# Optimization experiments

Hardware: AMD Instinct MI355X
Metric: run time of the kernel (lower is better)

## Reference

```python
import jax, jax.numpy as jnp
import numpy as np

DECAY = 0.99
EPS = 1e-10
COMMIT = 0.25
K = 1024
D = 64


def setup_inputs() -> dict:
    key = jax.random.key(0)
    k1, k2, k3, k4 = jax.random.split(key, 4)
    return {
        "z_e": jax.random.normal(k1, (64, 64, 32, 32), dtype=jnp.float32),
        "embedding_w": jax.random.normal(k2, (K, D), dtype=jnp.float32),
        "ema_cluster_size": jax.random.uniform(k3, (K,), dtype=jnp.float32),
        "ema_w": jax.random.normal(k4, (K, D), dtype=jnp.float32),
    }


def reference(z_e, embedding_w, ema_cluster_size, ema_w):
    # [B, C, H, W] -> [B, H, W, C] -> [N, D]
    z_nhwc = jnp.transpose(z_e, (0, 2, 3, 1))
    z_flat = z_nhwc.reshape(-1, z_nhwc.shape[-1])

    # Squared-euclidean distances via ||z||^2 + ||e||^2 - 2 z e^T  -> [N, K]
    z_sq = jnp.sum(z_flat * z_flat, axis=1, keepdims=True)
    e_sq = jnp.sum(embedding_w * embedding_w, axis=1)
    distances = z_sq + e_sq - 2.0 * (z_flat @ embedding_w.T)

    indices = jnp.argmin(distances, axis=1)                      # [N]
    encodings = jax.nn.one_hot(indices, K, dtype=z_flat.dtype)   # [N, K]

    quantized = embedding_w[indices].reshape(z_nhwc.shape)       # [B, H, W, C]

    # --- EMA codebook update (training path; no-grad in original) ---
    counts = jnp.sum(encodings, axis=0)                          # [K]
    new_cluster_size = DECAY * ema_cluster_size + (1.0 - DECAY) * counts
    dw = encodings.T @ z_flat                                    # [K, D]
    new_ema_w = DECAY * ema_w + (1.0 - DECAY) * dw
    n = jnp.sum(new_cluster_size)
    cluster_size = (new_cluster_size + EPS) / (n + K * EPS) * n
    new_embedding_w = new_ema_w / cluster_size[:, None]

    # Commitment loss (quantized detached)
    diff = jax.lax.stop_gradient(quantized) - z_nhwc
    loss = COMMIT * jnp.mean(diff * diff)

    # Straight-through estimator
    quantized_st = z_nhwc + jax.lax.stop_gradient(quantized - z_nhwc)

    avg_probs = jnp.mean(encodings, axis=0)
    perplexity = jnp.exp(-jnp.sum(avg_probs * jnp.log(avg_probs + 1e-10)))

    quantized_out = jnp.transpose(quantized_st, (0, 3, 1, 2))    # [B, C, H, W]
    return (quantized_out, loss, perplexity, encodings,
            new_embedding_w, new_cluster_size, new_ema_w)
```

## Files before the change

### kernel.cpp

```cpp
#include <hip/hip_runtime.h>
#include <math.h>

#define NTOT 65536
#define KCB  1024
#define DIM  64

typedef float fvec2 __attribute__((ext_vector_type(2)));
typedef float fvec4 __attribute__((ext_vector_type(4)));
typedef short sh8  __attribute__((ext_vector_type(8)));

static const size_t OFF_Q    = 0;
static const size_t OFF_LOSS = 4194304;
static const size_t OFF_PERP = 4194305;
static const size_t OFF_ENC  = 4194306;
static const size_t OFF_EMB  = 71303170;
static const size_t OFF_NCS  = 71368706;
static const size_t OFF_NEMA = 71369730;

static const size_t WSO_IDX   = 0;
static const size_t WSO_ESQ   = 262144;
static const size_t WSO_LOSSP = 266240;
static const size_t WSO_CNT   = 270336;
static const size_t WSO_SCAL  = 274432;
static const size_t WSO_EBH   = 278528;
static const size_t WSO_EBL   = 409600;
static const size_t WSO_ZC    = 540672;
static const size_t WS_NEED_ZC = 540672 + (size_t)NTOT * DIM * 4;

__device__ __forceinline__ unsigned short f2bf(float f) {
    unsigned u = __builtin_bit_cast(unsigned, f);
    return (unsigned short)((u + 0x7FFFu + ((u >> 16) & 1u)) >> 16);
}
__device__ __forceinline__ float bf2f(unsigned short h) {
    unsigned u = ((unsigned)h) << 16;
    return __builtin_bit_cast(float, u);
}

__global__ void k_eprep(const float* __restrict__ emb,
                        unsigned short* __restrict__ ebh,
                        unsigned short* __restrict__ ebl,
                        float* __restrict__ esq) {
    int gid = blockIdx.x * 256 + threadIdx.x;
    int c = gid >> 3, ko8 = gid & 7;
    const fvec4* p = (const fvec4*)(emb + ((size_t)c << 6) + (ko8 << 3));
    fvec4 v0 = p[0], v1 = p[1];
    float f[8] = {v0.x, v0.y, v0.z, v0.w, v1.x, v1.y, v1.z, v1.w};
    sh8 h, l;
    float sq0 = 0.f, sq1 = 0.f;
#pragma unroll
    for (int j = 0; j < 8; ++j) {
        unsigned short hb = f2bf(f[j]);
        h[j] = (short)hb;
        l[j] = (short)f2bf(f[j] - bf2f(hb));
        if (j < 4) sq0 = fmaf(f[j], f[j], sq0); else sq1 = fmaf(f[j], f[j], sq1);
    }
    float sq = sq0 + sq1;
    sq += __shfl_xor(sq, 1, 64);
    sq += __shfl_xor(sq, 2, 64);
    sq += __shfl_xor(sq, 4, 64);
    if (ko8 == 0) esq[c] = sq;

    int ct = c >> 4, cl = c & 15, kc = ko8 >> 2, ko = ko8 & 3;
    size_t base = ((((size_t)ct << 1) + kc) << 9) + (((size_t)(ko << 4) + cl) << 3);
    *(sh8*)(ebh + base) = h;
    *(sh8*)(ebl + base) = l;
}

__global__ __launch_bounds__(256, 4)
void k_assign(const float* __restrict__ ze, const float* __restrict__ emb,
              const float* __restrict__ esq,
              const unsigned short* __restrict__ ebh,
              const unsigned short* __restrict__ ebl,
              int* __restrict__ idx_out, float* __restrict__ lossp,
              float* __restrict__ zc, int use_zc) {
    __shared__ float zt[4096];
    __shared__ __align__(16) float etq[4096];
    __shared__ int   sfidx[64];

    const int tid  = threadIdx.x;
    const int blk  = blockIdx.x;
    const int b    = blk >> 4;
    const int hw0  = (blk & 15) << 6;
    const int n0   = blk << 6;
    const int lane = tid & 63;
    const int wave = tid >> 6;
    const int cg   = lane & 15;
    const int ko   = lane >> 4;

    char*  ebuf0 = (char*)etq;
    char*  ebuf1 = (char*)etq + 4096;
    float* esql  = etq + 2048;

#pragma unroll
    for (int j = 0; j < 4; ++j) {
        int idx = tid + (j << 8);
        int d = idx >> 4, r0 = (idx & 15) << 2;
        const fvec4 v = *(const fvec4*)(ze + (((size_t)(b << 6) + d) << 10) + hw0 + r0);
        zt[(r0 + 0) * 64 + d] = v.x;
        zt[(r0 + 1) * 64 + d] = v.y;
        zt[(r0 + 2) * 64 + d] = v.z;
        zt[(r0 + 3) * 64 + d] = v.w;
    }
    {
        fvec4 e4 = *(const fvec4*)(esq + (tid << 2));
        *(fvec4*)&esql[tid << 2] = e4;
    }

    const unsigned short* sgbase = (tid < 128) ? ebh : ebl;
    const int soff   = (tid & 127) << 3;
    const int dstoff = (tid < 128) ? (tid << 4) : (2048 + ((tid - 128) << 4));
    const size_t lo  = (size_t)lane << 4;

#define TILE(i) ((((i) + (blk << 1)) & 63))

    sh8 stg = *(const sh8*)(sgbase + ((size_t)TILE(0) << 10) + soff);
    __syncthreads();

    const int arow = (wave << 4) + cg;
    sh8 Ah0, Ah1, Al0, Al1;
#pragma unroll
    for (int j = 0; j < 8; ++j) {
        float f0 = zt[arow * 64 + (ko << 3) + j];
        float f1 = zt[arow * 64 + 32 + (ko << 3) + j];
        unsigned short h0 = f2bf(f0), h1 = f2bf(f1);
        Ah0[j] = (short)h0;  Al0[j] = (short)f2bf(f0 - bf2f(h0));
        Ah1[j] = (short)h1;  Al1[j] = (short)f2bf(f1 - bf2f(h1));
    }

    *(sh8*)(ebuf0 + dstoff) = stg;
    __syncthreads();

    float tb[4]  = {3.4e38f, 3.4e38f, 3.4e38f, 3.4e38f};
    float ts2[4] = {3.4e38f, 3.4e38f, 3.4e38f, 3.4e38f};
    int ti1[4] = {0, 0, 0, 0};
    int ti2[4] = {0, 0, 0, 0};

    for (int i = 0; i < 64; ++i) {
        const int ct = TILE(i);
        const char* rb = (i & 1) ? ebuf1 : ebuf0;
        char*       wb = (i & 1) ? ebuf0 : ebuf1;
        if (i < 63)
            stg = *(const sh8*)(sgbase + ((size_t)TILE(i + 1) << 10) + soff);

        sh8 bh0 = *(const sh8*)(rb + lo);
        sh8 bh1 = *(const sh8*)(rb + 1024 + lo);
        sh8 bl0 = *(const sh8*)(rb + 2048 + lo);
        sh8 bl1 = *(const sh8*)(rb + 3072 + lo);

        fvec4 aa = {0.f, 0.f, 0.f, 0.f}, ab = {0.f, 0.f, 0.f, 0.f};
        aa = __builtin_amdgcn_mfma_f32_16x16x32_bf16(Ah0, bh0, aa, 0, 0, 0);
        ab = __builtin_amdgcn_mfma_f32_16x16x32_bf16(Ah1, bh1, ab, 0, 0, 0);
        aa = __builtin_amdgcn_mfma_f32_16x16x32_bf16(Ah0, bl0, aa, 0, 0, 0);
        ab = __builtin_amdgcn_mfma_f32_16x16x32_bf16(Ah1, bl1, ab, 0, 0, 0);
        aa = __builtin_amdgcn_mfma_f32_16x16x32_bf16(Al0, bh0, aa, 0, 0, 0);
        ab = __builtin_amdgcn_mfma_f32_16x16x32_bf16(Al1, bh1, ab, 0, 0, 0);
        fvec4 acc = aa + ab;

        const int code = (ct << 4) + cg;
        const float es = esql[code];
#pragma unroll
        for (int rg = 0; rg < 4; ++rg) {
            float s = fmaf(acc[rg], -2.0f, es);
            bool c1 = s < tb[rg];
            bool c2 = s < ts2[rg];
            ti2[rg] = c1 ? ti1[rg] : (c2 ? code : ti2[rg]);
            ts2[rg] = c1 ? tb[rg] : (c2 ? s : ts2[rg]);
            ti1[rg] = c1 ? code : ti1[rg];
            tb[rg]  = c1 ? s : tb[rg];
        }

        if (i < 63) *(sh8*)(wb + dstoff) = stg;
        __syncthreads();
    }
#undef TILE

    float* mb  = etq;
    float* ms2 = etq + 1024;
    int*   mi1 = (int*)(etq + 2048);
    int*   mi2 = (int*)(etq + 3072);
#pragma unroll
    for (int rg = 0; rg < 4; ++rg) {
        int row = (wave << 4) + (ko << 2) + rg;
        mb [(cg << 6) + row] = tb[rg];
        ms2[(cg << 6) + row] = ts2[rg];
        mi1[(cg << 6) + row] = ti1[rg];
        mi2[(cg << 6) + row] = ti2[rg];
    }
    __syncthreads();

    if (tid < 64) {
        const int r = tid;
        float fb = mb[r], fs2 = ms2[r];
        int fi1 = mi1[r], fi2 = mi2[r];
#pragma unroll
        for (int p = 1; p < 16; ++p) {
            float ob = mb[(p << 6) + r], os2 = ms2[(p << 6) + r];
            int oi1 = mi1[(p << 6) + r], oi2 = mi2[(p << 6) + r];
            if (ob < fb)       { fs2 = fb; fi2 = fi1; fb = ob; fi1 = oi1; }
            else if (ob < fs2) { fs2 = ob; fi2 = oi1; }
            if (os2 < fs2)     { fs2 = os2; fi2 = oi2; }
        }
        if (fs2 - fb < 2e-2f) {
            double d1 = 0.0, d2 = 0.0;
            const float* e1 = emb + (size_t)fi1 * 64;
            const float* e2 = emb + (size_t)fi2 * 64;
            for (int d = 0; d < 64; ++d) {
                double zd = (double)zt[r * 64 + d];
                double q1 = zd - (double)e1[d];
                double q2 = zd - (double)e2[d];
                d1 += q1 * q1;
                d2 += q2 * q2;
            }
            if ((d2 < d1) || (d2 == d1 && fi2 < fi1)) fi1 = fi2;
        }
        sfidx[r] = fi1;
        idx_out[n0 + r] = fi1;
    }
    __syncthreads();

    float lacc = 0.f;
    for (int i = tid; i < 1024; i += 256) {
        int r = i >> 4, d4 = (i & 15) << 2;
        const fvec4 zv = *(const fvec4*)&zt[(r << 6) + d4];
        const fvec4 ev = *(const fvec4*)(emb + ((size_t)sfidx[r] << 6) + d4);
        fvec4 df = ev - zv;
        lacc = fmaf(df.x, df.x, lacc);
        lacc = fmaf(df.y, df.y, lacc);
        lacc = fmaf(df.z, df.z, lacc);
        lacc = fmaf(df.w, df.w, lacc);
        if (use_zc)
            *(fvec4*)&zc[(((size_t)(n0 + r)) << 6) + d4] = zv;
    }
    __syncthreads();

    float* lred = etq;
    lred[tid] = lacc;
    __syncthreads();
    for (int s = 128; s > 0; s >>= 1) {
        if (tid < s) lred[tid] += lred[tid + s];
        __syncthreads();
    }
    if (tid == 0) lossp[blk] = lred[0];
}

__global__ __launch_bounds__(256)
void k_tail(const int* __restrict__ idx, const float* __restrict__ zcmp,
            const float* __restrict__ ze, const float* __restrict__ emaw,
            const float* __restrict__ ecs, const float* __restrict__ emb,
            float* __restrict__ out, int* __restrict__ counts, int use_zc) {
    __shared__ __align__(16) char smem[17424];
    const int t = threadIdx.x;

    if (blockIdx.x & 1) {
        const int blk = blockIdx.x >> 1;
        const int b   = blk >> 4;
        const int hw0 = (blk & 15) << 6;
        const int n0  = blk << 6;
        int*   sfidx = (int*)smem;
        float* qt    = (float*)(smem + 256);

        if (t < 64) sfidx[t] = idx[n0 + t];
        __syncthreads();

        for (int i = t; i < 4096; i += 256) {
            int r = i >> 6, d = i & 63;
            qt[d * 65 + r] = emb[(size_t)sfidx[r] * 64 + d];
        }

        float* ebase = out + OFF_ENC;
        if (t < 255) {
            const int cb = 2 + (t << 2);
            for (int r = 0; r < 64; ++r) {
                const int fi = sfidx[r];
                fvec4 v;
                v.x = (fi == cb)     ? 1.0f : 0.0f;
                v.y = (fi == cb + 1) ? 1.0f : 0.0f;
                v.z = (fi == cb + 2) ? 1.0f : 0.0f;
                v.w = (fi == cb + 3) ? 1.0f : 0.0f;
                __builtin_nontemporal_store(
                    v, (fvec4*)(ebase + ((size_t)(n0 + r) << 10) + cb));
            }
        } else {
            for (int r = 0; r < 64; ++r) {
                const int fi = sfidx[r];
                float* rowp = ebase + ((size_t)(n0 + r) << 10);
                fvec2 hd, tl;
                hd.x = (fi == 0)    ? 1.0f : 0.0f;
                hd.y = (fi == 1)    ? 1.0f : 0.0f;
                tl.x = (fi == 1022) ? 1.0f : 0.0f;
                tl.y = (fi == 1023) ? 1.0f : 0.0f;
                __builtin_nontemporal_store(hd, (fvec2*)rowp);
                __builtin_nontemporal_store(tl, (fvec2*)(rowp + 1022));
            }
        }
        __syncthreads();

        for (int i = t; i < 4096; i += 256) {
            int d = i >> 6, r = i & 63;
            __builtin_nontemporal_store(
                qt[d * 65 + r],
                &out[OFF_Q + ((size_t)((b << 6) + d) << 10) + hw0 + r]);
        }
        return;
    }

    const int k    = blockIdx.x >> 1;
    const int g    = t >> 6;
    const int d    = t & 63;
    const int lane = t & 63;
    int*   s_list = (int*)smem;
    int*   s_wsum = (int*)(smem + 16384);
    float* s_red  = (float*)(smem + 16400);

#define ZLOAD(n) (use_zc ? zcmp[((size_t)(n) << 6) + d] \
                         : ze[((((size_t)((n) >> 10) << 6) + d) << 10) + ((n) & 1023)])

    float a0 = 0.f, a1 = 0.f, a2 = 0.f, a3 = 0.f;
    int totalM = 0;

    for (int chunk = 0; chunk < 16; ++chunk) {
        const int base = chunk << 12;
        const int nb   = base + (t << 4);
        const int4* ip = (const int4*)(idx + nb);
        const int4 v0 = ip[0], v1 = ip[1], v2 = ip[2], v3 = ip[3];

        int c = 0;
        c += (v0.x == k) + (v0.y == k) + (v0.z == k) + (v0.w == k);
        c += (v1.x == k) + (v1.y == k) + (v1.z == k) + (v1.w == k);
        c += (v2.x == k) + (v2.y == k) + (v2.z == k) + (v2.w == k);
        c += (v3.x == k) + (v3.y == k) + (v3.z == k) + (v3.w == k);

        int inc = c;
#pragma unroll
        for (int off = 1; off < 64; off <<= 1) {
            int y = __shfl_up(inc, (unsigned)off, 64);
            if (lane >= off) inc += y;
        }
        if (lane == 63) s_wsum[g] = inc;
        __syncthreads();

        int wbase = 0;
#pragma unroll
        for (int w = 0; w < 4; ++w) wbase += (w < g) ? s_wsum[w] : 0;
        const int M = s_wsum[0] + s_wsum[1] + s_wsum[2] + s_wsum[3];
        int pos = wbase + inc - c;

        if (v0.x == k) s_list[pos++] = nb + 0;
        if (v0.y == k) s_list[pos++] = nb + 1;
        if (v0.z == k) s_list[pos++] = nb + 2;
        if (v0.w == k) s_list[pos++] = nb + 3;
        if (v1.x == k) s_list[pos++] = nb + 4;
        if (v1.y == k) s_list[pos++] = nb + 5;
        if (v1.z == k) s_list[pos++] = nb + 6;
        if (v1.w == k) s_list[pos++] = nb + 7;
        if (v2.x == k) s_list[pos++] = nb + 8;
        if (v2.y == k) s_list[pos++] = nb + 9;
        if (v2.z == k) s_list[pos++] = nb + 10;
        if (v2.w == k) s_list[pos++] = nb + 11;
        if (v3.x == k) s_list[pos++] = nb + 12;
        if (v3.y == k) s_list[pos++] = nb + 13;
        if (v3.z == k) s_list[pos++] = nb + 14;
        if (v3.w == k) s_list[pos++] = nb + 15;
        __syncthreads();

        int j = g;
        for (; j + 12 < M; j += 16) {
            int n0_ = s_list[j], n1_ = s_list[j + 4];
            int n2_ = s_list[j + 8], n3_ = s_list[j + 12];
            float z0 = ZLOAD(n0_), z1 = ZLOAD(n1_);
            float z2 = ZLOAD(n2_), z3 = ZLOAD(n3_);
            a0 += z0; a1 += z1; a2 += z2; a3 += z3;
        }
        for (; j < M; j += 4) a0 += ZLOAD(s_list[j]);
        totalM += M;
        __syncthreads();
    }
#undef ZLOAD

    s_red[(g << 6) + d] = (a0 + a1) + (a2 + a3);
    __syncthreads();
    if (g == 0) {
        float s = ((s_red[d] + s_red[64 + d]) + s_red[128 + d]) + s_red[192 + d];
        out[OFF_NEMA + ((size_t)k << 6) + d] =
            fmaf(0.01f, s, 0.99f * emaw[((size_t)k << 6) + d]);
    }
    if (t == 0) {
        counts[k] = totalM;
        out[OFF_NCS + k] = fmaf(0.01f, (float)totalM, 0.99f * ecs[k]);
    }
}

__global__ void k_scalars(const float* __restrict__ lossp, const int* __restrict__ counts,
                          const float* __restrict__ ncs, float* __restrict__ out,
                          float* __restrict__ scal) {
    __shared__ float sr[256];
    const int t = threadIdx.x;

    float v = lossp[t] + lossp[t + 256] + lossp[t + 512] + lossp[t + 768];
    sr[t] = v;
    __syncthreads();
    for (int s = 128; s > 0; s >>= 1) { if (t < s) sr[t] += sr[t + s]; __syncthreads(); }
    if (t == 0) out[OFF_LOSS] = sr[0] * (0.25f / 4194304.0f);
    __syncthreads();

    v = ncs[t] + ncs[t + 256] + ncs[t + 512] + ncs[t + 768];
    sr[t] = v;
    __syncthreads();
    for (int s = 128; s > 0; s >>= 1) { if (t < s) sr[t] += sr[t + s]; __syncthreads(); }
    if (t == 0) scal[0] = sr[0];
    __syncthreads();

    float pv = 0.f;
    for (int i = t; i < 1024; i += 256) {
        float p = (float)counts[i] * (1.0f / 65536.0f);
        pv += p * logf(p + 1e-10f);
    }
    sr[t] = pv;
    __syncthreads();
    for (int s = 128; s > 0; s >>= 1) { if (t < s) sr[t] += sr[t + s]; __syncthreads(); }
    if (t == 0) out[OFF_PERP] = expf(-sr[0]);
}

__global__ void k_embnorm(const float* __restrict__ nema, const float* __restrict__ ncs,
                          const float* __restrict__ scal, float* __restrict__ embw) {
    int i = blockIdx.x * 256 + threadIdx.x;
    float n = scal[0];
    int k = i >> 6;
    float cs = (ncs[k] + 1e-10f) / (n + 1.024e-7f) * n;
    embw[i] = nema[i] / cs;
}

extern "C" void kernel_launch(void* const* d_in, const int* in_sizes, int n_in,
                              void* d_out, int out_size, void* d_ws, size_t ws_size,
                              hipStream_t stream) {
    const float* ze   = (const float*)d_in[0];
    const float* emb  = (const float*)d_in[1];
    const float* ecs  = (const float*)d_in[2];
    const float* emaw = (const float*)d_in[3];
    float* out = (float*)d_out;
    char*  ws  = (char*)d_ws;

    int*            idx    = (int*)(ws + WSO_IDX);
    float*          esq    = (float*)(ws + WSO_ESQ);
    float*          lossp  = (float*)(ws + WSO_LOSSP);
    int*            counts = (int*)(ws + WSO_CNT);
    float*          scal   = (float*)(ws + WSO_SCAL);
    unsigned short* ebh    = (unsigned short*)(ws + WSO_EBH);
    unsigned short* ebl    = (unsigned short*)(ws + WSO_EBL);
    float*          zc     = (float*)(ws + WSO_ZC);
    const int use_zc = (ws_size >= WS_NEED_ZC) ? 1 : 0;

    k_eprep  <<<32,   256, 0, stream>>>(emb, ebh, ebl, esq);
    k_assign <<<1024, 256, 0, stream>>>(ze, emb, esq, ebh, ebl, idx, lossp, zc, use_zc);
    k_tail   <<<2048, 256, 0, stream>>>(idx, zc, ze, emaw, ecs, emb, out, counts, use_zc);
    k_scalars<<<1,    256, 0, stream>>>(lossp, counts, out + OFF_NCS, out, scal);
    k_embnorm<<<256,  256, 0, stream>>>(out + OFF_NEMA, out + OFF_NCS, scal, out + OFF_EMB);
}
```

Before: 164.6 us.

## Stage four codebook tiles per barrier in assign kernel

The assign kernel's main loop now loads four codebook tiles into shared memory per iteration instead of double-buffering one tile at a time. This cuts the barrier count from 64 to 32 and lets more work run between syncs. The next group's global loads are issued after the barrier so they overlap the MFMAs. In exchange it holds four staging registers per thread, uses a larger shared allocation (16 KB buffer plus a separate esq array), and drops double buffering, so each group's shared write must wait for the previous compute to finish.

```diff
diff --git a/kernel.cpp b/kernel.cpp
--- a/kernel.cpp
+++ b/kernel.cpp
@@ -74,7 +74,8 @@
               int* __restrict__ idx_out, float* __restrict__ lossp,
               float* __restrict__ zc, int use_zc) {
     __shared__ float zt[4096];
-    __shared__ __align__(16) float etq[4096];
+    __shared__ __align__(16) float ebuf[4096];
+    __shared__ float esql[1024];
     __shared__ int   sfidx[64];
 
     const int tid  = threadIdx.x;
@@ -87,10 +88,6 @@
     const int cg   = lane & 15;
     const int ko   = lane >> 4;
 
-    char*  ebuf0 = (char*)etq;
-    char*  ebuf1 = (char*)etq + 4096;
-    float* esql  = etq + 2048;
-
 #pragma unroll
     for (int j = 0; j < 4; ++j) {
         int idx = tid + (j << 8);
@@ -107,13 +104,16 @@
     }
 
     const unsigned short* sgbase = (tid < 128) ? ebh : ebl;
-    const int soff   = (tid & 127) << 3;
-    const int dstoff = (tid < 128) ? (tid << 4) : (2048 + ((tid - 128) << 4));
-    const size_t lo  = (size_t)lane << 4;
-
-#define TILE(i) ((((i) + (blk << 1)) & 63))
-
-    sh8 stg = *(const sh8*)(sgbase + ((size_t)TILE(0) << 10) + soff);
+    const int  soff = (tid & 127) << 3;
+    const int  dstw = ((tid & 127) << 2) + ((tid < 128) ? 0 : 512);
+    char* ebc = (char*)ebuf;
+
+#define TILE(i) ((((i) + (blk << 2)) & 63))
+
+    sh8 st0 = *(const sh8*)(sgbase + ((size_t)TILE(0) << 10) + soff);
+    sh8 st1 = *(const sh8*)(sgbase + ((size_t)TILE(1) << 10) + soff);
+    sh8 st2 = *(const sh8*)(sgbase + ((size_t)TILE(2) << 10) + soff);
+    sh8 st3 = *(const sh8*)(sgbase + ((size_t)TILE(3) << 10) + soff);
     __syncthreads();
 
     const int arow = (wave << 4) + cg;
@@ -127,57 +127,65 @@
         Ah1[j] = (short)h1;  Al1[j] = (short)f2bf(f1 - bf2f(h1));
     }
 
-    *(sh8*)(ebuf0 + dstoff) = stg;
-    __syncthreads();
-
     float tb[4]  = {3.4e38f, 3.4e38f, 3.4e38f, 3.4e38f};
     float ts2[4] = {3.4e38f, 3.4e38f, 3.4e38f, 3.4e38f};
     int ti1[4] = {0, 0, 0, 0};
     int ti2[4] = {0, 0, 0, 0};
 
-    for (int i = 0; i < 64; ++i) {
-        const int ct = TILE(i);
-        const char* rb = (i & 1) ? ebuf1 : ebuf0;
-        char*       wb = (i & 1) ? ebuf0 : ebuf1;
-        if (i < 63)
-            stg = *(const sh8*)(sgbase + ((size_t)TILE(i + 1) << 10) + soff);
-
-        sh8 bh0 = *(const sh8*)(rb + lo);
-        sh8 bh1 = *(const sh8*)(rb + 1024 + lo);
-        sh8 bl0 = *(const sh8*)(rb + 2048 + lo);
-        sh8 bl1 = *(const sh8*)(rb + 3072 + lo);
-
-        fvec4 aa = {0.f, 0.f, 0.f, 0.f}, ab = {0.f, 0.f, 0.f, 0.f};
-        aa = __builtin_amdgcn_mfma_f32_16x16x32_bf16(Ah0, bh0, aa, 0, 0, 0);
-        ab = __builtin_amdgcn_mfma_f32_16x16x32_bf16(Ah1, bh1, ab, 0, 0, 0);
-        aa = __builtin_amdgcn_mfma_f32_16x16x32_bf16(Ah0, bl0, aa, 0, 0, 0);
-        ab = __builtin_amdgcn_mfma_f32_16x16x32_bf16(Ah1, bl1, ab, 0, 0, 0);
-        aa = __builtin_amdgcn_mfma_f32_16x16x32_bf16(Al0, bh0, aa, 0, 0, 0);
-        ab = __builtin_amdgcn_mfma_f32_16x16x32_bf16(Al1, bh1, ab, 0, 0, 0);
-        fvec4 acc = aa + ab;
-
-        const int code = (ct << 4) + cg;
-        const float es = esql[code];
-#pragma unroll
-        for (int rg = 0; rg < 4; ++rg) {
-            float s = fmaf(acc[rg], -2.0f, es);
-            bool c1 = s < tb[rg];
-            bool c2 = s < ts2[rg];
-            ti2[rg] = c1 ? ti1[rg] : (c2 ? code : ti2[rg]);
-            ts2[rg] = c1 ? tb[rg] : (c2 ? s : ts2[rg]);
-            ti1[rg] = c1 ? code : ti1[rg];
-            tb[rg]  = c1 ? s : tb[rg];
-        }
-
-        if (i < 63) *(sh8*)(wb + dstoff) = stg;
+    for (int g = 0; g < 16; ++g) {
+        *(sh8*)&ebuf[dstw]        = st0;
+        *(sh8*)&ebuf[1024 + dstw] = st1;
+        *(sh8*)&ebuf[2048 + dstw] = st2;
+        *(sh8*)&ebuf[3072 + dstw] = st3;
+        __syncthreads();
+
+        if (g < 15) {
+            const int i4 = (g << 2) + 4;
+            st0 = *(const sh8*)(sgbase + ((size_t)TILE(i4 + 0) << 10) + soff);
+            st1 = *(const sh8*)(sgbase + ((size_t)TILE(i4 + 1) << 10) + soff);
+            st2 = *(const sh8*)(sgbase + ((size_t)TILE(i4 + 2) << 10) + soff);
+            st3 = *(const sh8*)(sgbase + ((size_t)TILE(i4 + 3) << 10) + soff);
+        }
+
+#pragma unroll
+        for (int s = 0; s < 4; ++s) {
+            const int ct = TILE((g << 2) + s);
+            const char* sb = ebc + (s << 12);
+            sh8 bh0 = *(const sh8*)(sb + (lane << 4));
+            sh8 bh1 = *(const sh8*)(sb + 1024 + (lane << 4));
+            sh8 bl0 = *(const sh8*)(sb + 2048 + (lane << 4));
+            sh8 bl1 = *(const sh8*)(sb + 3072 + (lane << 4));
+
+            fvec4 aa = {0.f, 0.f, 0.f, 0.f}, ab = {0.f, 0.f, 0.f, 0.f};
+            aa = __builtin_amdgcn_mfma_f32_16x16x32_bf16(Ah0, bh0, aa, 0, 0, 0);
+            ab = __builtin_amdgcn_mfma_f32_16x16x32_bf16(Ah1, bh1, ab, 0, 0, 0);
+            aa = __builtin_amdgcn_mfma_f32_16x16x32_bf16(Ah0, bl0, aa, 0, 0, 0);
+            ab = __builtin_amdgcn_mfma_f32_16x16x32_bf16(Ah1, bl1, ab, 0, 0, 0);
+            aa = __builtin_amdgcn_mfma_f32_16x16x32_bf16(Al0, bh0, aa, 0, 0, 0);
+            ab = __builtin_amdgcn_mfma_f32_16x16x32_bf16(Al1, bh1, ab, 0, 0, 0);
+            fvec4 acc = aa + ab;
+
+            const int code = (ct << 4) + cg;
+            const float es = esql[code];
+#pragma unroll
+            for (int rg = 0; rg < 4; ++rg) {
+                float s_ = fmaf(acc[rg], -2.0f, es);
+                bool c1 = s_ < tb[rg];
+                bool c2 = s_ < ts2[rg];
+                ti2[rg] = c1 ? ti1[rg] : (c2 ? code : ti2[rg]);
+                ts2[rg] = c1 ? tb[rg] : (c2 ? s_ : ts2[rg]);
+                ti1[rg] = c1 ? code : ti1[rg];
+                tb[rg]  = c1 ? s_ : tb[rg];
+            }
+        }
         __syncthreads();
     }
 #undef TILE
 
-    float* mb  = etq;
-    float* ms2 = etq + 1024;
-    int*   mi1 = (int*)(etq + 2048);
-    int*   mi2 = (int*)(etq + 3072);
+    float* mb  = ebuf;
+    float* ms2 = ebuf + 1024;
+    int*   mi1 = (int*)(ebuf + 2048);
+    int*   mi2 = (int*)(ebuf + 3072);
 #pragma unroll
     for (int rg = 0; rg < 4; ++rg) {
         int row = (wave << 4) + (ko << 2) + rg;
@@ -233,7 +241,7 @@
     }
     __syncthreads();
 
-    float* lred = etq;
+    float* lred = ebuf;
     lred[tid] = lacc;
     __syncthreads();
     for (int s = 128; s > 0; s >>= 1) {
```

New measurement: 155.3 us. 1.06x faster.
